# Kernel optimization log

Measured on AMD Instinct MI355X. Metric: run time of the kernel, lower is better.

## Reference

```python
import jax, jax.numpy as jnp
import numpy as np
import math

MODEL_DIM = 2048
NUM_EXPERTS = 64
N_TOKENS = 16384
CAPACITY_FACTOR = 1.0
MIN_CAPACITY = 8
THRESHOLD = 0.5


def _threshold_gating(logits):
    # Faithful jax translation of main_thresholdGating (training path, threshold>0).
    # Note: the torch code truncates sorted columns to the data-dependent
    # explore_top_k_num; we keep the full E columns instead. This is exactly
    # equivalent: dropped columns are all-unchosen (importance 0), and using
    # arange(E,0,-1) instead of arange(K,0,-1) shifts every chosen importance
    # by the same constant (E-K), which preserves the per-expert top-k order.
    N, E = logits.shape
    capacity = max(int(math.ceil(N / E * CAPACITY_FACTOR)), MIN_CAPACITY)  # static

    gates = jax.nn.softmax(logits, axis=1)                    # [N,E]
    indices1 = jnp.argmax(gates, axis=1)                      # top-1 expert per token
    mask1 = jax.nn.one_hot(indices1, E, dtype=gates.dtype)    # [N,E]

    # sorted gates + cumsum threshold selection
    gates_sorted, gates_idx = jax.lax.top_k(gates, E)         # [N,E] descending
    cum = jnp.cumsum(gates_sorted, axis=-1)
    chosen = (cum - gates_sorted) < THRESHOLD                 # [N,E] bool
    chosen = chosen.at[:, 0].set(True)                        # always keep top-1

    # scatter importance = rank-priority + gate prob into expert columns
    rank_imp = jnp.arange(E, 0, -1, dtype=gates.dtype)[None, :] + gates_sorted
    imp = jnp.where(chosen, rank_imp, jnp.zeros_like(rank_imp))
    row = jnp.arange(N)[:, None]
    # gates_idx rows are permutations of experts -> no scatter collisions
    tam = jnp.zeros((N, E), gates.dtype).at[row, gates_idx].set(imp)  # [N,E]

    # capacity truncation: per expert column keep the `capacity` tokens with
    # highest importance
    top_idx = jax.lax.top_k(tam.T, capacity)[1]               # [E, capacity]
    keep = jnp.zeros((N, E), gates.dtype).at[top_idx, jnp.arange(E)[:, None]].set(1.0)
    final_mask = ((tam * keep) > 0).astype(gates.dtype)       # [N,E]

    combine_weights = gates * final_mask

    # load-balancing aux loss (GShard style)
    me = jnp.mean(gates, axis=0)
    ce = jnp.mean(mask1, axis=0)
    l_aux = jnp.sum(me * ce) * E
    return l_aux, combine_weights


def setup_inputs() -> dict:
    key = jax.random.key(0)
    kx, kw = jax.random.split(key)
    x = jax.random.normal(kx, (N_TOKENS, MODEL_DIM), dtype=jnp.float32)
    # gate weight of wg = Linear(model_dim, num_experts, bias=False)
    W = jax.random.normal(kw, (NUM_EXPERTS, MODEL_DIM), dtype=jnp.float32) / math.sqrt(MODEL_DIM)
    return {"x": x, "W": W}


def reference(x, W):
    logits = x @ W.T                                          # [N,E]
    l_aux, combine_weights = _threshold_gating(logits)
    return l_aux, combine_weights
```

## Files before the change

kernel.cpp:

```cpp
#include <hip/hip_runtime.h>
#include <cstdint>
#include <cstddef>

#define N_TOK  16384
#define NEXP   64
#define KDIM   2048
#define CAP    256
#define NE_TOT ((size_t)N_TOK * NEXP)

typedef __attribute__((ext_vector_type(8))) short short8;
typedef __attribute__((ext_vector_type(4))) float f32x4;
typedef __attribute__((ext_vector_type(4))) unsigned int uint4x;

__device__ __forceinline__ unsigned short bf16_rtn(float f) {
  unsigned u = __float_as_uint(f);
  u += 0x7FFFu + ((u >> 16) & 1u);
  return (unsigned short)(u >> 16);
}
__device__ __forceinline__ float bf16_f(unsigned short h) {
  return __uint_as_float((unsigned)h << 16);
}
__device__ __forceinline__ f32x4 MF(short8 a, short8 b, f32x4 c) {
  return __builtin_amdgcn_mfma_f32_16x16x32_bf16(a, b, c, 0, 0, 0);
}
__device__ __forceinline__ unsigned cvt_pk(float a, float b) {
  unsigned r;
  asm("v_cvt_pk_bf16_f32 %0, %1, %2" : "=v"(r) : "v"(a), "v"(b));
  return r;
}
__device__ __forceinline__ float lo16f(unsigned u) {
  return __uint_as_float(u << 16);
}
__device__ __forceinline__ float hi16f(unsigned u) {
  return __uint_as_float(u & 0xFFFF0000u);
}

__global__ __launch_bounds__(256) void wdigits(const float* __restrict__ W,
    unsigned short* __restrict__ Wh, unsigned short* __restrict__ Wl,
    unsigned short* __restrict__ Wq) {
  const int e = (int)blockIdx.x * 256 + (int)threadIdx.x;
  const int col = e >> 11;
  const int k   = e & 2047;
  const float w = W[(size_t)col * KDIM + k];
  const unsigned short h = bf16_rtn(w);
  const float r1 = w - bf16_f(h);
  const unsigned short lo = bf16_rtn(r1);
  const float r2 = r1 - bf16_f(lo);
  const unsigned short q = bf16_rtn(r2);
  const size_t idx = (size_t)(k >> 3) * 512 + (size_t)col * 8 + (k & 7);
  Wh[idx] = h; Wl[idx] = lo; Wq[idx] = q;
}

__device__ __forceinline__ void cvt8pk(float4 a, float4 b,
                                       short8& h, short8& lo, short8& q) {
  const float f0 = a.x, f1 = a.y, f2 = a.z, f3 = a.w;
  const float f4 = b.x, f5 = b.y, f6 = b.z, f7 = b.w;
  const unsigned h0 = cvt_pk(f0, f1), h1 = cvt_pk(f2, f3);
  const unsigned h2 = cvt_pk(f4, f5), h3 = cvt_pk(f6, f7);
  const float r0 = f0 - lo16f(h0), r1 = f1 - hi16f(h0);
  const float r2 = f2 - lo16f(h1), r3 = f3 - hi16f(h1);
  const float r4 = f4 - lo16f(h2), r5 = f5 - hi16f(h2);
  const float r6 = f6 - lo16f(h3), r7 = f7 - hi16f(h3);
  const unsigned l0 = cvt_pk(r0, r1), l1 = cvt_pk(r2, r3);
  const unsigned l2 = cvt_pk(r4, r5), l3 = cvt_pk(r6, r7);
  const float s0 = r0 - lo16f(l0), s1 = r1 - hi16f(l0);
  const float s2 = r2 - lo16f(l1), s3 = r3 - hi16f(l1);
  const float s4 = r4 - lo16f(l2), s5 = r5 - hi16f(l2);
  const float s6 = r6 - lo16f(l3), s7 = r7 - hi16f(l3);
  const unsigned q0 = cvt_pk(s0, s1), q1 = cvt_pk(s2, s3);
  const unsigned q2 = cvt_pk(s4, s5), q3 = cvt_pk(s6, s7);
  h  = __builtin_bit_cast(short8, (uint4x){h0, h1, h2, h3});
  lo = __builtin_bit_cast(short8, (uint4x){l0, l1, l2, l3});
  q  = __builtin_bit_cast(short8, (uint4x){q0, q1, q2, q3});
}

template <int KS>
__global__ __launch_bounds__(256) void gemm_mfma(const float* __restrict__ x,
    const unsigned short* __restrict__ Wh, const unsigned short* __restrict__ Wl,
    const unsigned short* __restrict__ Wq, float* __restrict__ part) {
  constexpr int NSTEP = (KDIM / KS) / 32;
  const int tid = (int)threadIdx.x;
  const int l   = tid & 63;
  const int wv  = tid >> 6;
  const int ks  = (int)blockIdx.x >> 8;
  const int mt  = (((int)blockIdx.x & 255) << 2) + wv;
  const int row0 = mt * 16;
  const int kBeg = ks * (KDIM / KS);
  const int lr = l & 15;
  const int lk = l >> 4;

  f32x4 acc0 = {0.f,0.f,0.f,0.f}, acc1 = {0.f,0.f,0.f,0.f};
  f32x4 acc2 = {0.f,0.f,0.f,0.f}, acc3 = {0.f,0.f,0.f,0.f};

  const float* pa = x + (size_t)(row0 + lr) * KDIM + kBeg + lk * 8;
  const size_t bbase = ((size_t)((kBeg >> 3) + lk)) * 64 + lr;
  const short8* BH = (const short8*)Wh + bbase;
  const short8* BL = (const short8*)Wl + bbase;
  const short8* BQ = (const short8*)Wq + bbase;

  float4 A0 = *(const float4*)pa;
  float4 A1 = *(const float4*)(pa + 4);
  short8 bh = BH[0], bl = BL[0], bq = BQ[0];

  for (int s = 0; s < NSTEP; ++s) {
    const int so = s * 256;
    float4 N0, N1;
    if (s + 1 < NSTEP) {
      pa += 32;
      N0 = *(const float4*)pa;
      N1 = *(const float4*)(pa + 4);
    }
    short8 a_h, a_l, a_q;
    cvt8pk(A0, A1, a_h, a_l, a_q);

#define CT_BLOCK(ACC)                                   \
    ACC = MF(a_h, bh, ACC); ACC = MF(a_h, bl, ACC);     \
    ACC = MF(a_l, bh, ACC); ACC = MF(a_l, bl, ACC);     \
    ACC = MF(a_q, bh, ACC); ACC = MF(a_h, bq, ACC);

    short8 nh, nl, nq;
    nh = BH[so + 16]; nl = BL[so + 16]; nq = BQ[so + 16];
    CT_BLOCK(acc0)
    bh = nh; bl = nl; bq = nq;
    nh = BH[so + 32]; nl = BL[so + 32]; nq = BQ[so + 32];
    CT_BLOCK(acc1)
    bh = nh; bl = nl; bq = nq;
    nh = BH[so + 48]; nl = BL[so + 48]; nq = BQ[so + 48];
    CT_BLOCK(acc2)
    bh = nh; bl = nl; bq = nq;
    const int ni = (s + 1 < NSTEP) ? so + 256 : so;
    nh = BH[ni]; nl = BL[ni]; nq = BQ[ni];
    CT_BLOCK(acc3)
    bh = nh; bl = nl; bq = nq;
#undef CT_BLOCK

    if (s + 1 < NSTEP) { A0 = N0; A1 = N1; }
  }

  float* pout = part + (size_t)ks * NE_TOT;
  const int rb = row0 + lk * 4;
#pragma unroll
  for (int r = 0; r < 4; ++r) {
    pout[(size_t)(rb + r) * 64 +  0 + lr] = acc0[r];
    pout[(size_t)(rb + r) * 64 + 16 + lr] = acc1[r];
    pout[(size_t)(rb + r) * 64 + 32 + lr] = acc2[r];
    pout[(size_t)(rb + r) * 64 + 48 + lr] = acc3[r];
  }
}

template <int KS>
__global__ __launch_bounds__(1024) void gate_rows(const float* __restrict__ part,
                                                  float* __restrict__ gatesT,
                                                  float* __restrict__ tamT) {
  __shared__ float gt[64][65];
  __shared__ float tt[64][65];
  const int tid  = (int)threadIdx.x;
  const int lane = tid & 63;
  const int wid  = tid >> 6;
  const int row0 = (int)blockIdx.x * 64;

#pragma unroll
  for (int r = 0; r < 4; ++r) {
    const int rloc = wid * 4 + r;
    const size_t base = (size_t)(row0 + rloc) * NEXP;

    float logit = 0.f;
#pragma unroll
    for (int s = 0; s < KS; ++s)
      logit += part[(size_t)s * NE_TOT + base + lane];

    float m = logit;
#pragma unroll
    for (int off = 32; off > 0; off >>= 1) m = fmaxf(m, __shfl_xor(m, off));
    float p = expf(logit - m);
    float sum = p;
#pragma unroll
    for (int off = 32; off > 0; off >>= 1) sum += __shfl_xor(sum, off);
    const float gate = p / sum;

    float g = gate;
    int idx = lane;
#pragma unroll
    for (int k = 2; k <= 64; k <<= 1) {
#pragma unroll
      for (int j = k >> 1; j > 0; j >>= 1) {
        float og = __shfl_xor(g, j);
        int   oi = __shfl_xor(idx, j);
        bool iLower     = (lane & j) == 0;
        bool wantFirst  = ((lane & k) == 0) ? iLower : !iLower;
        bool otherFirst = (og > g) || (og == g && oi < idx);
        if (otherFirst == wantFirst) { g = og; idx = oi; }
      }
    }

    float cum = g;
#pragma unroll
    for (int off = 1; off < 64; off <<= 1) {
      float t = __shfl_up(cum, off);
      if (lane >= off) cum += t;
    }
    const bool chosen = (lane == 0) || ((cum - g) < 0.5f);
    const float imp = chosen ? ((float)(NEXP - lane) + g) : 0.f;

    gt[rloc][lane] = gate;
    tt[rloc][idx]  = imp;
  }
  __syncthreads();

#pragma unroll
  for (int p = 0; p < 4; ++p) {
    const int e = p * 16 + wid;
    gatesT[(size_t)e * N_TOK + row0 + lane] = gt[lane][e];
    tamT  [(size_t)e * N_TOK + row0 + lane] = tt[lane][e];
  }
}

__global__ __launch_bounds__(1024) void expert_select(
    const float* __restrict__ gatesT, const float* __restrict__ tamT,
    float* __restrict__ me_sum, int* __restrict__ ce_cnt,
    float* __restrict__ combT) {
  __shared__ int   hist16[16][256];
  __shared__ int   hist[256];
  __shared__ float wsum[16];
  __shared__ int   wice[16];
  __shared__ int   wnnz[16];
  __shared__ int   wcnt[16];
  __shared__ unsigned sh_prefix;
  __shared__ int      sh_k;
  __shared__ int      sh_nnz;

  const int e    = (int)blockIdx.x;
  const int tid  = (int)threadIdx.x;
  const int lane = tid & 63;
  const int wid  = tid >> 6;
  const float* tcol = tamT   + (size_t)e * N_TOK;
  const float* gcol = gatesT + (size_t)e * N_TOK;

  float gsum = 0.f;
  int ccnt = 0, nnzl = 0;
#pragma unroll
  for (int k = 0; k < 4; ++k) {
    int i4 = tid + k * 1024;
    float4 tv = reinterpret_cast<const float4*>(tcol)[i4];
    float4 gv = reinterpret_cast<const float4*>(gcol)[i4];
    gsum += gv.x + gv.y + gv.z + gv.w;
    ccnt += (tv.x > 64.f) + (tv.y > 64.f) + (tv.z > 64.f) + (tv.w > 64.f);
    nnzl += (tv.x != 0.f) + (tv.y != 0.f) + (tv.z != 0.f) + (tv.w != 0.f);
  }
#pragma unroll
  for (int off = 32; off > 0; off >>= 1) {
    gsum += __shfl_xor(gsum, off);
    ccnt += __shfl_xor(ccnt, off);
    nnzl += __shfl_xor(nnzl, off);
  }
  if (lane == 0) { wsum[wid] = gsum; wice[wid] = ccnt; wnnz[wid] = nnzl; }
  __syncthreads();
  if (tid == 0) {
    float t = 0.f; int c = 0, nz = 0;
    for (int w = 0; w < 16; ++w) { t += wsum[w]; c += wice[w]; nz += wnnz[w]; }
    me_sum[e] = t; ce_cnt[e] = c; sh_nnz = nz;
  }
  __syncthreads();
  const int nnz = sh_nnz;

  unsigned vstar = 0u;
  int meq = 0;
  if (nnz > CAP) {
    unsigned prefix = 0;
    int krem = CAP;
    for (int round = 0; round < 4; ++round) {
      const int shift = 24 - 8 * round;
      const unsigned maskAbove =
          (round == 0) ? 0u : (0xFFFFFFFFu << (shift + 8));
      for (int z = tid; z < 16 * 256; z += 1024) ((int*)hist16)[z] = 0;
      __syncthreads();
#pragma unroll
      for (int k = 0; k < 16; ++k) {
        unsigned u = __float_as_uint(tcol[tid + k * 1024]);
        if (u != 0u && (u & maskAbove) == prefix)
          atomicAdd(&hist16[wid][(u >> shift) & 255], 1);
      }
      __syncthreads();
      if (tid < 256) {
        int s = 0;
#pragma unroll
        for (int w = 0; w < 16; ++w) s += hist16[w][tid];
        hist[tid] = s;
      }
      __syncthreads();
      if (wid == 0) {
        int h0 = hist[lane * 4 + 0], h1 = hist[lane * 4 + 1];
        int h2 = hist[lane * 4 + 2], h3 = hist[lane * 4 + 3];
        int lsum = h0 + h1 + h2 + h3;
        int suf = lsum;
#pragma unroll
        for (int off = 1; off < 64; off <<= 1) {
          int t = __shfl_down(suf, off);
          if (lane + off < 64) suf += t;
        }
        int above = suf - lsum;
        int S3 = above + h3, S2 = S3 + h2, S1 = S2 + h1, S0 = S1 + h0;
        if (S0 >= krem && S1    < krem) { sh_prefix = prefix | ((unsigned)(lane*4+0) << shift); sh_k = krem - S1;    }
        if (S1 >= krem && S2    < krem) { sh_prefix = prefix | ((unsigned)(lane*4+1) << shift); sh_k = krem - S2;    }
        if (S2 >= krem && S3    < krem) { sh_prefix = prefix | ((unsigned)(lane*4+2) << shift); sh_k = krem - S3;    }
        if (S3 >= krem && above < krem) { sh_prefix = prefix | ((unsigned)(lane*4+3) << shift); sh_k = krem - above; }
      }
      __syncthreads();
      prefix = sh_prefix;
      krem   = sh_k;
      __syncthreads();
    }
    vstar = prefix;
    meq   = krem;
  }

  float4 tq[4];
#pragma unroll
  for (int q = 0; q < 4; ++q)
    tq[q] = reinterpret_cast<const float4*>(tcol)[tid * 4 + q];
  int cnt = 0;
#pragma unroll
  for (int q = 0; q < 4; ++q) {
    cnt += (__float_as_uint(tq[q].x) == vstar);
    cnt += (__float_as_uint(tq[q].y) == vstar);
    cnt += (__float_as_uint(tq[q].z) == vstar);
    cnt += (__float_as_uint(tq[q].w) == vstar);
  }
  int inc = cnt;
#pragma unroll
  for (int off = 1; off < 64; off <<= 1) {
    int t = __shfl_up(inc, off);
    if (lane >= off) inc += t;
  }
  if (lane == 63) wcnt[wid] = inc;
  __syncthreads();
  if (tid == 0) {
    int run = 0;
    for (int w = 0; w < 16; ++w) { int t = wcnt[w]; wcnt[w] = run; run += t; }
  }
  __syncthreads();
  int exc = (inc - cnt) + wcnt[wid];

  float* ccol = combT + (size_t)e * N_TOK;
#pragma unroll
  for (int q = 0; q < 4; ++q) {
    float4 gq = reinterpret_cast<const float4*>(gcol)[tid * 4 + q];
    float ov[4];
    const float tv[4] = {tq[q].x, tq[q].y, tq[q].z, tq[q].w};
    const float gv[4] = {gq.x, gq.y, gq.z, gq.w};
#pragma unroll
    for (int j = 0; j < 4; ++j) {
      unsigned u = __float_as_uint(tv[j]);
      bool keep;
      if (u == vstar) { keep = (exc < meq); ++exc; }
      else            { keep = (u > vstar); }
      ov[j] = (keep && u != 0u) ? gv[j] : 0.f;
    }
    reinterpret_cast<float4*>(ccol)[tid * 4 + q] =
        make_float4(ov[0], ov[1], ov[2], ov[3]);
  }
}

__global__ __launch_bounds__(1024) void transpose_out(
    const float* __restrict__ combT, float* __restrict__ out1,
    const float* __restrict__ me_sum, const int* __restrict__ ce_cnt,
    float* __restrict__ out0) {
  __shared__ float tile[64][65];
  const int tid  = (int)threadIdx.x;
  const int lane = tid & 63;
  const int wid  = tid >> 6;
  const int tok0 = (int)blockIdx.x * 64;
#pragma unroll
  for (int p = 0; p < 4; ++p) {
    const int e = p * 16 + wid;
    tile[lane][e] = combT[(size_t)e * N_TOK + tok0 + lane];
  }
  __syncthreads();
#pragma unroll
  for (int q = 0; q < 4; ++q) {
    const int tok = q * 16 + wid;
    out1[(size_t)(tok0 + tok) * NEXP + lane] = tile[tok][lane];
  }
  if (blockIdx.x == 0 && wid == 0) {
    float v = (me_sum[lane] / (float)N_TOK) *
              ((float)ce_cnt[lane] / (float)N_TOK);
#pragma unroll
    for (int off = 32; off > 0; off >>= 1) v += __shfl_xor(v, off);
    if (lane == 0) out0[0] = v * (float)NEXP;
  }
}

extern "C" void kernel_launch(void* const* d_in, const int* in_sizes, int n_in,
                              void* d_out, int out_size, void* d_ws, size_t ws_size,
                              hipStream_t stream) {
  const float* x = (const float*)d_in[0];
  const float* W = (const float*)d_in[1];
  float* out = (float*)d_out;
  float* ws  = (float*)d_ws;

  const bool ks8 = ws_size >= (size_t)(8 + 2) * NE_TOT * 4 + 1024;
  const int  KS  = ks8 ? 8 : 4;

  float* part   = ws;
  float* combT  = ws;
  float* gatesT = ws + (size_t)KS * NE_TOT;
  float* tamT   = gatesT + NE_TOT;
  float* me     = tamT + NE_TOT;
  int*   ce     = (int*)(me + 64);

  unsigned short* Wh = (unsigned short*)gatesT;
  unsigned short* Wl = Wh + (size_t)NEXP * KDIM;
  unsigned short* Wq = Wl + (size_t)NEXP * KDIM;

  wdigits<<<(NEXP * KDIM) / 256, 256, 0, stream>>>(W, Wh, Wl, Wq);
  if (ks8) gemm_mfma<8><<<256 * 8, 256, 0, stream>>>(x, Wh, Wl, Wq, part);
  else     gemm_mfma<4><<<256 * 4, 256, 0, stream>>>(x, Wh, Wl, Wq, part);
  if (ks8) gate_rows<8><<<N_TOK / 64, 1024, 0, stream>>>(part, gatesT, tamT);
  else     gate_rows<4><<<N_TOK / 64, 1024, 0, stream>>>(part, gatesT, tamT);
  expert_select<<<NEXP, 1024, 0, stream>>>(gatesT, tamT, me, ce, combT);
  transpose_out<<<N_TOK / 64, 1024, 0, stream>>>(combT, out + 1, me, ce, out);
}
```

Baseline: 87.35 us.

## Stage x tiles through LDS with async global_load_lds double buffering

The GEMM kernel now loads each wave's 16x32 fp32 slice of x into a per-wave, XOR-swizzled LDS double buffer using global_load_lds, and waits with vmcnt so the next slice's load overlaps compute on the current one. The B-operand loads are also restructured: all twelve fragments for a step are loaded up front and the MFMAs are interleaved across the four accumulators instead of running as four sequential chains. The aim is coalesced x loads and hidden memory latency, plus less MFMA dependency stalling. In exchange it adds LDS use, more live registers, and relies on hand-written waitcnt ordering being correct.

```diff
diff --git a/kernel.cpp b/kernel.cpp
--- a/kernel.cpp
+++ b/kernel.cpp
@@ -79,63 +79,73 @@
     const unsigned short* __restrict__ Wh, const unsigned short* __restrict__ Wl,
     const unsigned short* __restrict__ Wq, float* __restrict__ part) {
   constexpr int NSTEP = (KDIM / KS) / 32;
+  __shared__ float xs[4][2][512];
   const int tid = (int)threadIdx.x;
   const int l   = tid & 63;
-  const int wv  = tid >> 6;
+  const int wid = tid >> 6;
   const int ks  = (int)blockIdx.x >> 8;
-  const int mt  = (((int)blockIdx.x & 255) << 2) + wv;
-  const int row0 = mt * 16;
+  const int mt  = (int)blockIdx.x & 255;
+  const int row0 = mt * 64 + wid * 16;
   const int kBeg = ks * (KDIM / KS);
   const int lr = l & 15;
   const int lk = l >> 4;
 
-  f32x4 acc0 = {0.f,0.f,0.f,0.f}, acc1 = {0.f,0.f,0.f,0.f};
-  f32x4 acc2 = {0.f,0.f,0.f,0.f}, acc3 = {0.f,0.f,0.f,0.f};
-
-  const float* pa = x + (size_t)(row0 + lr) * KDIM + kBeg + lk * 8;
+  const int srow = l >> 3;
+  const int scol = ((l & 7) * 4) ^ ((srow & 7) << 2);
+  const float* sp0 = x + (size_t)(row0 + srow)     * KDIM + kBeg + scol;
+  const float* sp1 = x + (size_t)(row0 + 8 + srow) * KDIM + kBeg + scol;
+
+  const int rsw = (lr & 7) << 2;
+  const float* rp0 = &xs[wid][0][lr * 32 + ((lk * 8)     ^ rsw)];
+  const float* rp1 = &xs[wid][0][lr * 32 + ((lk * 8 + 4) ^ rsw)];
+
   const size_t bbase = ((size_t)((kBeg >> 3) + lk)) * 64 + lr;
   const short8* BH = (const short8*)Wh + bbase;
   const short8* BL = (const short8*)Wl + bbase;
   const short8* BQ = (const short8*)Wq + bbase;
 
-  float4 A0 = *(const float4*)pa;
-  float4 A1 = *(const float4*)(pa + 4);
-  short8 bh = BH[0], bl = BL[0], bq = BQ[0];
+  f32x4 acc0 = {0.f,0.f,0.f,0.f}, acc1 = {0.f,0.f,0.f,0.f};
+  f32x4 acc2 = {0.f,0.f,0.f,0.f}, acc3 = {0.f,0.f,0.f,0.f};
+
+#define STAGE(buf, koff)                                                     \
+  __builtin_amdgcn_global_load_lds((const float*)(sp0 + (koff)),             \
+                                   &xs[wid][(buf)][0],   16, 0, 0);          \
+  __builtin_amdgcn_global_load_lds((const float*)(sp1 + (koff)),             \
+                                   &xs[wid][(buf)][256], 16, 0, 0);
+
+  STAGE(0, 0)
 
   for (int s = 0; s < NSTEP; ++s) {
-    const int so = s * 256;
-    float4 N0, N1;
-    if (s + 1 < NSTEP) {
-      pa += 32;
-      N0 = *(const float4*)pa;
-      N1 = *(const float4*)(pa + 4);
-    }
+    const int cur = s & 1;
+    const int nk = (s + 1 < NSTEP) ? (s + 1) * 32 : 0;
+    if (cur == 0) { STAGE(1, nk) } else { STAGE(0, nk) }
+    asm volatile("s_waitcnt vmcnt(2)" ::: "memory");
+
+    float4 A0 = *(const float4*)(rp0 + cur * 512);
+    float4 A1 = *(const float4*)(rp1 + cur * 512);
+
     short8 a_h, a_l, a_q;
     cvt8pk(A0, A1, a_h, a_l, a_q);
 
-#define CT_BLOCK(ACC)                                   \
-    ACC = MF(a_h, bh, ACC); ACC = MF(a_h, bl, ACC);     \
-    ACC = MF(a_l, bh, ACC); ACC = MF(a_l, bl, ACC);     \
-    ACC = MF(a_q, bh, ACC); ACC = MF(a_h, bq, ACC);
-
-    short8 nh, nl, nq;
-    nh = BH[so + 16]; nl = BL[so + 16]; nq = BQ[so + 16];
-    CT_BLOCK(acc0)
-    bh = nh; bl = nl; bq = nq;
-    nh = BH[so + 32]; nl = BL[so + 32]; nq = BQ[so + 32];
-    CT_BLOCK(acc1)
-    bh = nh; bl = nl; bq = nq;
-    nh = BH[so + 48]; nl = BL[so + 48]; nq = BQ[so + 48];
-    CT_BLOCK(acc2)
-    bh = nh; bl = nl; bq = nq;
-    const int ni = (s + 1 < NSTEP) ? so + 256 : so;
-    nh = BH[ni]; nl = BL[ni]; nq = BQ[ni];
-    CT_BLOCK(acc3)
-    bh = nh; bl = nl; bq = nq;
-#undef CT_BLOCK
-
-    if (s + 1 < NSTEP) { A0 = N0; A1 = N1; }
-  }
+    const int so = s * 256;
+    short8 bh0 = BH[so +  0], bh1 = BH[so + 16], bh2 = BH[so + 32], bh3 = BH[so + 48];
+    short8 bl0 = BL[so +  0], bl1 = BL[so + 16], bl2 = BL[so + 32], bl3 = BL[so + 48];
+    short8 bq0 = BQ[so +  0], bq1 = BQ[so + 16], bq2 = BQ[so + 32], bq3 = BQ[so + 48];
+
+    acc0 = MF(a_h, bh0, acc0); acc1 = MF(a_h, bh1, acc1);
+    acc2 = MF(a_h, bh2, acc2); acc3 = MF(a_h, bh3, acc3);
+    acc0 = MF(a_h, bl0, acc0); acc1 = MF(a_h, bl1, acc1);
+    acc2 = MF(a_h, bl2, acc2); acc3 = MF(a_h, bl3, acc3);
+    acc0 = MF(a_l, bh0, acc0); acc1 = MF(a_l, bh1, acc1);
+    acc2 = MF(a_l, bh2, acc2); acc3 = MF(a_l, bh3, acc3);
+    acc0 = MF(a_l, bl0, acc0); acc1 = MF(a_l, bl1, acc1);
+    acc2 = MF(a_l, bl2, acc2); acc3 = MF(a_l, bl3, acc3);
+    acc0 = MF(a_q, bh0, acc0); acc1 = MF(a_q, bh1, acc1);
+    acc2 = MF(a_q, bh2, acc2); acc3 = MF(a_q, bh3, acc3);
+    acc0 = MF(a_h, bq0, acc0); acc1 = MF(a_h, bq1, acc1);
+    acc2 = MF(a_h, bq2, acc2); acc3 = MF(a_h, bq3, acc3);
+  }
+#undef STAGE
 
   float* pout = part + (size_t)ks * NE_TOT;
   const int rb = row0 + lk * 4;
@@ -399,8 +409,8 @@
   float* ws  = (float*)d_ws;
 
   const bool ks8 = ws_size >= (size_t)(8 + 2) * NE_TOT * 4 + 1024;
-  const int  KS  = ks8 ? 8 : 4;
-
+
+  const int KS = ks8 ? 8 : 4;
   float* part   = ws;
   float* combT  = ws;
   float* gatesT = ws + (size_t)KS * NE_TOT;
```

New measurement: 87.66 us. Within noise of the previous version (+0.4%).

## Register-tile GEMM to 64 rows per wave, reusing B fragments across row tiles

Applied to the files above, without the earlier changes.

Each wave now computes four 16-row tiles (64 rows) instead of one, so the W digit fragments loaded per k-step are reused across four row tiles. The grid shrinks by a factor of four and blocks are ordered with the k-split index fastest. This cuts redundant loads of W, but it raises register pressure (64 accumulator floats plus staged A and B) and leaves fewer blocks to cover the GPU's compute units, which can hurt occupancy and latency hiding.

```diff
diff --git a/kernel.cpp b/kernel.cpp
--- a/kernel.cpp
+++ b/kernel.cpp
@@ -82,69 +82,86 @@
   const int tid = (int)threadIdx.x;
   const int l   = tid & 63;
   const int wv  = tid >> 6;
-  const int ks  = (int)blockIdx.x >> 8;
-  const int mt  = (((int)blockIdx.x & 255) << 2) + wv;
-  const int row0 = mt * 16;
+  const int ks  = (int)blockIdx.x % KS;
+  const int mt  = (int)blockIdx.x / KS;
+  const int row0 = mt * 256 + wv * 64;
   const int kBeg = ks * (KDIM / KS);
   const int lr = l & 15;
   const int lk = l >> 4;
 
-  f32x4 acc0 = {0.f,0.f,0.f,0.f}, acc1 = {0.f,0.f,0.f,0.f};
-  f32x4 acc2 = {0.f,0.f,0.f,0.f}, acc3 = {0.f,0.f,0.f,0.f};
-
-  const float* pa = x + (size_t)(row0 + lr) * KDIM + kBeg + lk * 8;
+  f32x4 acc[4][4];
+#pragma unroll
+  for (int rt = 0; rt < 4; ++rt)
+#pragma unroll
+    for (int cb = 0; cb < 4; ++cb) acc[rt][cb] = (f32x4){0.f, 0.f, 0.f, 0.f};
+
+  const float* pa0 = x + (size_t)(row0 + lr) * KDIM + kBeg + lk * 8;
   const size_t bbase = ((size_t)((kBeg >> 3) + lk)) * 64 + lr;
   const short8* BH = (const short8*)Wh + bbase;
   const short8* BL = (const short8*)Wl + bbase;
   const short8* BQ = (const short8*)Wq + bbase;
 
-  float4 A0 = *(const float4*)pa;
-  float4 A1 = *(const float4*)(pa + 4);
-  short8 bh = BH[0], bl = BL[0], bq = BQ[0];
+  float4 Ac[4][2];
+#pragma unroll
+  for (int rt = 0; rt < 4; ++rt) {
+    const float* p = pa0 + (size_t)rt * 16 * KDIM;
+    Ac[rt][0] = *(const float4*)p;
+    Ac[rt][1] = *(const float4*)(p + 4);
+  }
 
   for (int s = 0; s < NSTEP; ++s) {
     const int so = s * 256;
-    float4 N0, N1;
+    short8 bh[4], bl[4], bq[4];
+#pragma unroll
+    for (int cb = 0; cb < 4; ++cb) {
+      bh[cb] = BH[so + cb * 16];
+      bl[cb] = BL[so + cb * 16];
+      bq[cb] = BQ[so + cb * 16];
+    }
+    float4 An[4][2];
     if (s + 1 < NSTEP) {
-      pa += 32;
-      N0 = *(const float4*)pa;
-      N1 = *(const float4*)(pa + 4);
-    }
-    short8 a_h, a_l, a_q;
-    cvt8pk(A0, A1, a_h, a_l, a_q);
-
-#define CT_BLOCK(ACC)                                   \
-    ACC = MF(a_h, bh, ACC); ACC = MF(a_h, bl, ACC);     \
-    ACC = MF(a_l, bh, ACC); ACC = MF(a_l, bl, ACC);     \
-    ACC = MF(a_q, bh, ACC); ACC = MF(a_h, bq, ACC);
-
-    short8 nh, nl, nq;
-    nh = BH[so + 16]; nl = BL[so + 16]; nq = BQ[so + 16];
-    CT_BLOCK(acc0)
-    bh = nh; bl = nl; bq = nq;
-    nh = BH[so + 32]; nl = BL[so + 32]; nq = BQ[so + 32];
-    CT_BLOCK(acc1)
-    bh = nh; bl = nl; bq = nq;
-    nh = BH[so + 48]; nl = BL[so + 48]; nq = BQ[so + 48];
-    CT_BLOCK(acc2)
-    bh = nh; bl = nl; bq = nq;
-    const int ni = (s + 1 < NSTEP) ? so + 256 : so;
-    nh = BH[ni]; nl = BL[ni]; nq = BQ[ni];
-    CT_BLOCK(acc3)
-    bh = nh; bl = nl; bq = nq;
-#undef CT_BLOCK
-
-    if (s + 1 < NSTEP) { A0 = N0; A1 = N1; }
+      const int ko = (s + 1) * 32;
+#pragma unroll
+      for (int rt = 0; rt < 4; ++rt) {
+        const float* p = pa0 + (size_t)rt * 16 * KDIM + ko;
+        An[rt][0] = *(const float4*)p;
+        An[rt][1] = *(const float4*)(p + 4);
+      }
+    }
+    short8 ah[4], al[4], aq[4];
+#pragma unroll
+    for (int rt = 0; rt < 4; ++rt)
+      cvt8pk(Ac[rt][0], Ac[rt][1], ah[rt], al[rt], aq[rt]);
+
+#pragma unroll
+    for (int cb = 0; cb < 4; ++cb) {
+#pragma unroll
+      for (int rt = 0; rt < 4; ++rt) {
+        acc[rt][cb] = MF(ah[rt], bh[cb], acc[rt][cb]);
+        acc[rt][cb] = MF(ah[rt], bl[cb], acc[rt][cb]);
+        acc[rt][cb] = MF(al[rt], bh[cb], acc[rt][cb]);
+        acc[rt][cb] = MF(al[rt], bl[cb], acc[rt][cb]);
+        acc[rt][cb] = MF(aq[rt], bh[cb], acc[rt][cb]);
+        acc[rt][cb] = MF(ah[rt], bq[cb], acc[rt][cb]);
+      }
+    }
+
+    if (s + 1 < NSTEP) {
+#pragma unroll
+      for (int rt = 0; rt < 4; ++rt) { Ac[rt][0] = An[rt][0]; Ac[rt][1] = An[rt][1]; }
+    }
   }
 
   float* pout = part + (size_t)ks * NE_TOT;
-  const int rb = row0 + lk * 4;
-#pragma unroll
-  for (int r = 0; r < 4; ++r) {
-    pout[(size_t)(rb + r) * 64 +  0 + lr] = acc0[r];
-    pout[(size_t)(rb + r) * 64 + 16 + lr] = acc1[r];
-    pout[(size_t)(rb + r) * 64 + 32 + lr] = acc2[r];
-    pout[(size_t)(rb + r) * 64 + 48 + lr] = acc3[r];
+#pragma unroll
+  for (int rt = 0; rt < 4; ++rt) {
+    const int rb = row0 + rt * 16 + lk * 4;
+#pragma unroll
+    for (int r = 0; r < 4; ++r) {
+#pragma unroll
+      for (int cb = 0; cb < 4; ++cb)
+        pout[(size_t)(rb + r) * 64 + cb * 16 + lr] = acc[rt][cb][r];
+    }
   }
 }
 
@@ -399,8 +416,8 @@
   float* ws  = (float*)d_ws;
 
   const bool ks8 = ws_size >= (size_t)(8 + 2) * NE_TOT * 4 + 1024;
-  const int  KS  = ks8 ? 8 : 4;
-
+
+  const int KS = ks8 ? 8 : 4;
   float* part   = ws;
   float* combT  = ws;
   float* gatesT = ws + (size_t)KS * NE_TOT;
@@ -413,8 +430,8 @@
   unsigned short* Wq = Wl + (size_t)NEXP * KDIM;
 
   wdigits<<<(NEXP * KDIM) / 256, 256, 0, stream>>>(W, Wh, Wl, Wq);
-  if (ks8) gemm_mfma<8><<<256 * 8, 256, 0, stream>>>(x, Wh, Wl, Wq, part);
-  else     gemm_mfma<4><<<256 * 4, 256, 0, stream>>>(x, Wh, Wl, Wq, part);
+  if (ks8) gemm_mfma<8><<<64 * 8, 256, 0, stream>>>(x, Wh, Wl, Wq, part);
+  else     gemm_mfma<4><<<64 * 4, 256, 0, stream>>>(x, Wh, Wl, Wq, part);
   if (ks8) gate_rows<8><<<N_TOK / 64, 1024, 0, stream>>>(part, gatesT, tamT);
   else     gate_rows<4><<<N_TOK / 64, 1024, 0, stream>>>(part, gatesT, tamT);
   expert_select<<<NEXP, 1024, 0, stream>>>(gatesT, tamT, me, ce, combT);
```

Result: faster. 73.95 us (-15.3%).
